# Kernel tuning notes

Hardware: AMD Instinct MI355X
Metric: run time of the kernel (lower is better)

Reference implementation:

```python
import jax, jax.numpy as jnp
import numpy as np

NB, DM, DIN, DS, DTR, K = 4, 64, 128, 16, 4, 4
C, COUT, H, W, BATCH, NH = 256, 256, 32, 32, 4, 8


def layernorm(x, w, b, eps=1e-5):
    mu = x.mean(-1, keepdims=True)
    var = ((x - mu) ** 2).mean(-1, keepdims=True)
    return (x - mu) * jax.lax.rsqrt(var + eps) * w + b


def ln_hw(x, eps=1e-5):
    # F.layer_norm(x, [H, W]) -> normalize over last two dims, no affine
    mu = x.mean((-2, -1), keepdims=True)
    var = ((x - mu) ** 2).mean((-2, -1), keepdims=True)
    return (x - mu) * jax.lax.rsqrt(var + eps)


def conv1d(x, w, b, groups=1, pad=1):
    # x: (B, Cin, L), w: (Cout, Cin//groups, k)
    y = jax.lax.conv_general_dilated(x, w, (1,), [(pad, pad)],
                                     dimension_numbers=('NCH', 'OIH', 'NCH'),
                                     feature_group_count=groups)
    return y + b[None, :, None]


def selective_scan(u, dt, Bm, Cm, A, Dp):
    # u, dt: (B,L,din); Bm, Cm: (B,L,ds); A: (din,ds); Dp: (din,)
    dA = jnp.exp(dt[..., None] * A)                     # (B,L,din,ds)
    dBu = (dt * u)[..., None] * Bm[:, :, None, :]       # (B,L,din,ds)

    def step(h, inp):
        dA_t, dBu_t, C_t = inp
        h = dA_t * h + dBu_t
        return h, jnp.einsum('bds,bs->bd', h, C_t)

    h0 = jnp.zeros((u.shape[0], DIN, DS), u.dtype)
    _, ys = jax.lax.scan(step, h0, (dA.transpose(1, 0, 2, 3), dBu.transpose(1, 0, 2, 3), Cm.transpose(1, 0, 2)))
    return ys.transpose(1, 0, 2) + u * Dp


def mamba(xs, inw, convw, convb, xpw, dtw, dtb, alog, dp, outw):
    # xs: (B,L,DM) one branch of Mamba(d_model=DM, d_state=DS, d_conv=K, expand=2)
    xz = xs @ inw.T                                     # (B,L,2*DIN)
    u, z = jnp.split(xz, 2, axis=-1)
    # causal depthwise conv1d (torch pads K-1 and truncates to L == left pad K-1)
    uc = jax.lax.conv_general_dilated(u.transpose(0, 2, 1), convw[:, None, :], (1,), [(K - 1, 0)],
                                      dimension_numbers=('NCH', 'OIH', 'NCH'),
                                      feature_group_count=DIN) + convb[None, :, None]
    u = jax.nn.silu(uc.transpose(0, 2, 1))              # (B,L,DIN)
    xdbc = u @ xpw.T                                    # (B,L,DTR+2*DS)
    dt = jax.nn.softplus(xdbc[..., :DTR] @ dtw.T + dtb)
    Bm, Cm = xdbc[..., DTR:DTR + DS], xdbc[..., DTR + DS:]
    y = selective_scan(u, dt, Bm, Cm, -jnp.exp(alog), dp)
    return (y * jax.nn.silu(z)) @ outw.T


mamba_v = jax.vmap(mamba)  # over branch axis 0 of inputs and all params


def mha(x, inw, inb, outw, outb):
    B, N, Cc = x.shape
    hd = Cc // NH
    qkv = x @ inw.T + inb
    q, k, v = jnp.split(qkv, 3, axis=-1)
    q = q.reshape(B, N, NH, hd).transpose(0, 2, 1, 3)
    k = k.reshape(B, N, NH, hd).transpose(0, 2, 1, 3)
    v = v.reshape(B, N, NH, hd).transpose(0, 2, 1, 3)
    att = jax.nn.softmax((q @ k.transpose(0, 1, 3, 2)) * (1.0 / (hd ** 0.5)), axis=-1)
    o = (att @ v).transpose(0, 2, 1, 3).reshape(B, N, Cc)
    return o @ outw.T + outb


def reference(x, norm_w, norm_b, skip_scale, m_inw, m_convw, m_convb, m_xpw, m_dtw, m_dtb, m_alog, m_d, m_outw, qdw_w, qdw_b, qpw_w, qpw_b, rdw_w, rdw_b, rpw_w, rpw_b, fdw_w, fdw_b, fpw_w, fpw_b, lc_w, lc_b, attn_inw, attn_inb, attn_outw, attn_outb, lgn_w, lgn_b, fc_w, fc_b, dwc_w, dwc_b, proj_w, proj_b):
    B, Cc, Hh, Ww = x.shape
    N = Hh * Ww
    xs = x.reshape(B, Cc, N).transpose(0, 2, 1)         # (B,N,C)
    xn = layernorm(xs, norm_w, norm_b)
    # channel-chunk into NB branches: (NB,B,N,DM)
    xc = xn.reshape(B, N, NB, DM).transpose(2, 0, 1, 3)
    xm = mamba_v(xc, m_inw, m_convw, m_convb, m_xpw, m_dtw, m_dtb, m_alog, m_d, m_outw) + skip_scale * xc
    x_concat = xm.transpose(1, 2, 0, 3).reshape(B, N, Cc)
    # branch gating: depthwise grouped conv (C->NB) then pointwise (NB->NB)
    Q = conv1d(conv1d(x_concat.transpose(0, 2, 1), qdw_w, qdw_b, groups=NB, pad=1), qpw_w, qpw_b, groups=1, pad=0)
    g = jax.nn.sigmoid(Q)                               # (B,NB,N)
    xg = (g.transpose(1, 0, 2)[..., None] * xm).transpose(1, 2, 0, 3).reshape(B, N, Cc)
    xgt = xg.transpose(0, 2, 1)                          # (B,C,N)
    R = conv1d(conv1d(xgt, rdw_w, rdw_b, groups=Cc, pad=1), rpw_w, rpw_b, groups=1, pad=0) + xgt
    cat = jnp.concatenate([xs, R.transpose(0, 2, 1)], axis=-1).transpose(0, 2, 1)  # (B,2C,N)
    xm2 = conv1d(conv1d(cat, fdw_w, fdw_b, groups=2 * Cc, pad=1), fpw_w, fpw_b, groups=1, pad=0) + cat[:, :Cc, :]
    xm2 = xm2.transpose(0, 2, 1)                         # (B,N,C)
    # local-global feature mixing
    x_local = conv1d(xm2.transpose(0, 2, 1), lc_w, lc_b, groups=Cc, pad=1).transpose(0, 2, 1)
    x_global = mha(xm2, attn_inw, attn_inb, attn_outw, attn_outb)
    x_out = jnp.concatenate([x_local, x_global], axis=-1) @ fc_w.T + fc_b
    x_out = jax.nn.gelu(layernorm(x_out, lgn_w, lgn_b), approximate=False)
    # DepthwiseConvolution: layer_norm over [H,W] (no affine) then depthwise conv2d
    xi = x_out.transpose(0, 2, 1).reshape(B, Cc, Hh, Ww)
    xi = ln_hw(xi)
    xi = jax.lax.conv_general_dilated(xi, dwc_w, (1, 1), [(1, 1), (1, 1)],
                                      dimension_numbers=('NCHW', 'OIHW', 'NCHW'),
                                      feature_group_count=Cc) + dwc_b[None, :, None, None]
    x_mixed = xi.reshape(B, Cc, N).transpose(0, 2, 1)
    x_mixed = layernorm(x_mixed, norm_w, norm_b)        # self.norm reused
    x_mixed = x_mixed @ proj_w.T + proj_b
    return x_mixed.transpose(0, 2, 1).reshape(B, COUT, Hh, Ww)


def setup_inputs() -> dict:
    key = jax.random.key(0)
    ks = iter(jax.random.split(key, 64))

    def rn(shape, s=0.02):
        return jax.random.normal(next(ks), shape, jnp.float32) * s

    return dict(
        x=jax.random.normal(next(ks), (BATCH, C, H, W), jnp.float32),
        norm_w=jnp.ones((C,), jnp.float32), norm_b=jnp.zeros((C,), jnp.float32),
        skip_scale=jnp.ones((1,), jnp.float32),
        m_inw=rn((NB, 2 * DIN, DM)), m_convw=rn((NB, DIN, K), 0.2), m_convb=jnp.zeros((NB, DIN), jnp.float32),
        m_xpw=rn((NB, DTR + 2 * DS, DIN)), m_dtw=rn((NB, DIN, DTR), 0.2), m_dtb=rn((NB, DIN), 0.5),
        m_alog=jnp.tile(jnp.log(jnp.arange(1, DS + 1, dtype=jnp.float32)), (NB, DIN, 1)),
        m_d=jnp.ones((NB, DIN), jnp.float32), m_outw=rn((NB, DM, DIN)),
        qdw_w=rn((NB, C // NB, 3), 0.1), qdw_b=jnp.zeros((NB,), jnp.float32),
        qpw_w=rn((NB, NB, 1), 0.3), qpw_b=jnp.zeros((NB,), jnp.float32),
        rdw_w=rn((C, 1, 3), 0.2), rdw_b=jnp.zeros((C,), jnp.float32),
        rpw_w=rn((C, C, 1)), rpw_b=jnp.zeros((C,), jnp.float32),
        fdw_w=rn((2 * C, 1, 3), 0.2), fdw_b=jnp.zeros((2 * C,), jnp.float32),
        fpw_w=rn((C, 2 * C, 1)), fpw_b=jnp.zeros((C,), jnp.float32),
        lc_w=rn((C, 1, 3), 0.2), lc_b=jnp.zeros((C,), jnp.float32),
        attn_inw=rn((3 * C, C)), attn_inb=jnp.zeros((3 * C,), jnp.float32),
        attn_outw=rn((C, C)), attn_outb=jnp.zeros((C,), jnp.float32),
        lgn_w=jnp.ones((C,), jnp.float32), lgn_b=jnp.zeros((C,), jnp.float32),
        fc_w=rn((C, 2 * C)), fc_b=jnp.zeros((C,), jnp.float32),
        dwc_w=rn((C, 1, 3, 3), 0.2), dwc_b=jnp.zeros((C,), jnp.float32),
        proj_w=rn((COUT, C)), proj_b=jnp.zeros((COUT,), jnp.float32),
    )
```

## Files before the change

kernel.cpp:

```cpp
#include <hip/hip_runtime.h>
#include <math.h>


namespace {
constexpr int NB_ = 4, DM_ = 64, DIN_ = 128, DS_ = 16, DTR_ = 4;
constexpr int C_ = 256, N_ = 1024, B_ = 4, HD_ = 32;
constexpr int NCH = 16, LCH = 64;
constexpr int NSTATE = 16 * 128 * 16;
}

typedef __attribute__((ext_vector_type(8))) short bf16x8;
typedef __attribute__((ext_vector_type(4))) float f32x4;
typedef __attribute__((ext_vector_type(8))) unsigned short ushort8v;
typedef __attribute__((ext_vector_type(4))) unsigned short ushort4v;

__device__ __forceinline__ unsigned short f2b(float f) {
  unsigned int u = __float_as_uint(f);
  unsigned int r = u + 0x7FFFu + ((u >> 16) & 1u);
  return (unsigned short)(r >> 16);
}

__device__ __forceinline__ float2 blockReduce2(float a, float b, float* red) {
#pragma unroll
  for (int m = 1; m < 64; m <<= 1) {
    a += __shfl_xor(a, m, 64);
    b += __shfl_xor(b, m, 64);
  }
  int w = threadIdx.x >> 6;
  if ((threadIdx.x & 63) == 0) { red[2 * w] = a; red[2 * w + 1] = b; }
  __syncthreads();
  float ra = red[0] + red[2] + red[4] + red[6];
  float rb = red[1] + red[3] + red[5] + red[7];
  return make_float2(ra, rb);
}

__device__ __forceinline__ float siluf(float x) { return x / (1.f + expf(-x)); }
__device__ __forceinline__ float sigmf(float x) { return 1.f / (1.f + expf(-x)); }
__device__ __forceinline__ float softplusf(float x) {
  return fmaxf(x, 0.f) + log1pf(expf(-fabsf(x)));
}

__global__ __launch_bounds__(256) void k_ln_t2(const float* __restrict__ in,
                                               const float* __restrict__ w,
                                               const float* __restrict__ bias,
                                               float* __restrict__ out_ln,
                                               float* __restrict__ out_copy) {
  __shared__ float tile[256][17];
  __shared__ float redp[16][16][2];
  __shared__ float stats[16][2];
  int bx = blockIdx.x;
  int b = bx >> 6, n0 = (bx & 63) * 16;
  int c = threadIdx.x;
  {
    const float* p = in + ((long)(b * C_ + c)) * N_ + n0;
#pragma unroll
    for (int j = 0; j < 16; ++j) tile[c][j] = p[j];
  }
  __syncthreads();
  {
    int n = c & 15, g = c >> 4;
    float a = 0.f, q = 0.f;
#pragma unroll
    for (int i = 0; i < 16; ++i) {
      float v = tile[g * 16 + i][n];
      a += v; q += v * v;
    }
    redp[g][n][0] = a; redp[g][n][1] = q;
  }
  __syncthreads();
  if (c < 16) {
    float a = 0.f, q = 0.f;
#pragma unroll
    for (int g2 = 0; g2 < 16; ++g2) { a += redp[g2][c][0]; q += redp[g2][c][1]; }
    float mu = a * (1.f / C_);
    float rs = rsqrtf(q * (1.f / C_) - mu * mu + 1e-5f);
    stats[c][0] = mu; stats[c][1] = rs;
  }
  __syncthreads();
  float wv = w[c], bv = bias[c];
#pragma unroll
  for (int j = 0; j < 16; ++j) {
    float v = tile[c][j];
    long o = ((long)(b * N_ + n0 + j)) * C_ + c;
    if (out_copy) out_copy[o] = v;
    out_ln[o] = (v - stats[j][0]) * stats[j][1] * wv + bv;
  }
}

__global__ __launch_bounds__(256) void k_inproj_mfma(const float* __restrict__ xn,
                                                     const float* __restrict__ inw,
                                                     float* __restrict__ UPRE,
                                                     float* __restrict__ Z) {
  __shared__ unsigned short xa[64][72];
  __shared__ unsigned short wb[64][72];
  int r0 = blockIdx.x * 64;
  int nb = blockIdx.y >> 2, c0 = (blockIdx.y & 3) * 64;
  int t = threadIdx.x;
  int wv = t >> 6, lane = t & 63, g = lane >> 4, ql = lane & 15;
  const f32x4 zf = {0.f, 0.f, 0.f, 0.f};
  f32x4 acc[4] = {zf, zf, zf, zf};
  int rr = t >> 2, kq = (t & 3) * 16;
  {
    const float* xsrc = xn + (long)(r0 + rr) * C_ + nb * 64 + kq;
#pragma unroll
    for (int j = 0; j < 4; ++j) {
      float4 v = *(const float4*)(xsrc + 4 * j);
      ushort4v u = {f2b(v.x), f2b(v.y), f2b(v.z), f2b(v.w)};
      *(ushort4v*)&xa[rr][kq + 4 * j] = u;
    }
    const float* wsrc = inw + ((long)nb * 256 + c0 + rr) * 64 + kq;
#pragma unroll
    for (int j = 0; j < 4; ++j) {
      float4 v = *(const float4*)(wsrc + 4 * j);
      ushort4v u = {f2b(v.x), f2b(v.y), f2b(v.z), f2b(v.w)};
      *(ushort4v*)&wb[rr][kq + 4 * j] = u;
    }
  }
  __syncthreads();
#pragma unroll
  for (int ks = 0; ks < 2; ++ks) {
    bf16x8 a = *(const bf16x8*)&xa[wv * 16 + ql][ks * 32 + g * 8];
#pragma unroll
    for (int ct = 0; ct < 4; ++ct) {
      bf16x8 b = *(const bf16x8*)&wb[ct * 16 + ql][ks * 32 + g * 8];
      acc[ct] = __builtin_amdgcn_mfma_f32_16x16x32_bf16(a, b, acc[ct], 0, 0, 0);
    }
  }
#pragma unroll
  for (int ct = 0; ct < 4; ++ct) {
    int col = c0 + ct * 16 + ql;
#pragma unroll
    for (int reg = 0; reg < 4; ++reg) {
      long row = (long)nb * 4096 + r0 + wv * 16 + g * 4 + reg;
      if (col < 128) UPRE[row * DIN_ + col] = acc[ct][reg];
      else           Z[row * DIN_ + col - 128] = acc[ct][reg];
    }
  }
}

__global__ __launch_bounds__(256) void k_causal(const float* __restrict__ Uin,
                                                float* __restrict__ Uout,
                                                const float* __restrict__ cw,
                                                const float* __restrict__ cb) {
  __shared__ float u_s[35][128];
  int bx = blockIdx.x;
  int nbb = bx >> 5, chk = bx & 31;
  int nb = nbb >> 2;
  int n0 = chk * 32;
  const float* ibase = Uin + (long)nbb * N_ * DIN_;
  float* obase = Uout + (long)nbb * N_ * DIN_;
  for (int i = threadIdx.x; i < 35 * 32; i += 256) {
    int row = i >> 5, q = i & 31;
    int n = n0 - 3 + row;
    float4 v = (n >= 0) ? *(const float4*)&ibase[(long)n * DIN_ + q * 4]
                        : make_float4(0.f, 0.f, 0.f, 0.f);
    *(float4*)&u_s[row][q * 4] = v;
  }
  __syncthreads();
  int d = threadIdx.x & 127, half = threadIdx.x >> 7;
  float w0 = cw[(nb * DIN_ + d) * 4 + 0], w1 = cw[(nb * DIN_ + d) * 4 + 1];
  float w2 = cw[(nb * DIN_ + d) * 4 + 2], w3 = cw[(nb * DIN_ + d) * 4 + 3];
  float bv = cb[nb * DIN_ + d];
#pragma unroll
  for (int j = 0; j < 16; ++j) {
    int nn = half * 16 + j;
    float acc = bv + w3 * u_s[nn + 3][d] + w2 * u_s[nn + 2][d] +
                w1 * u_s[nn + 1][d] + w0 * u_s[nn][d];
    obase[(long)(n0 + nn) * DIN_ + d] = siluf(acc);
  }
}

__global__ __launch_bounds__(256) void k_xdbc_mfma(const float* __restrict__ U,
                                                   const float* __restrict__ xpw,
                                                   const float* __restrict__ dtw,
                                                   const float* __restrict__ dtb,
                                                   float* __restrict__ DT,
                                                   float* __restrict__ BMb,
                                                   float* __restrict__ CMb) {
  __shared__ unsigned short xa[64][72];
  __shared__ unsigned short wb[48][72];
  __shared__ float xd_s[64][40];
  __shared__ float dtw_s[128][4];
  __shared__ float dtb_s[128];
  int t = threadIdx.x;
  long row0 = (long)blockIdx.x * 64;
  int nb = blockIdx.x >> 6;
  for (int i = t; i < 512; i += 256) dtw_s[i >> 2][i & 3] = dtw[nb * 512 + i];
  if (t < 128) dtb_s[t] = dtb[nb * DIN_ + t];
  int wv = t >> 6, lane = t & 63, g = lane >> 4, ql = lane & 15;
  const f32x4 zf = {0.f, 0.f, 0.f, 0.f};
  f32x4 acc[3] = {zf, zf, zf};
  int rr = t >> 2, kq = (t & 3) * 16;
  for (int k0 = 0; k0 < 128; k0 += 64) {
    __syncthreads();
    const float* xsrc = U + (row0 + rr) * DIN_ + k0 + kq;
#pragma unroll
    for (int j = 0; j < 4; ++j) {
      float4 v = *(const float4*)(xsrc + 4 * j);
      ushort4v u = {f2b(v.x), f2b(v.y), f2b(v.z), f2b(v.w)};
      *(ushort4v*)&xa[rr][kq + 4 * j] = u;
    }
    if (rr < 48) {
      if (rr < 36) {
        const float* wsrc = xpw + (long)nb * 36 * 128 + rr * 128 + k0 + kq;
#pragma unroll
        for (int j = 0; j < 4; ++j) {
          float4 v = *(const float4*)(wsrc + 4 * j);
          ushort4v u = {f2b(v.x), f2b(v.y), f2b(v.z), f2b(v.w)};
          *(ushort4v*)&wb[rr][kq + 4 * j] = u;
        }
      } else {
        ushort4v z = {0, 0, 0, 0};
#pragma unroll
        for (int j = 0; j < 4; ++j) *(ushort4v*)&wb[rr][kq + 4 * j] = z;
      }
    }
    __syncthreads();
#pragma unroll
    for (int ks = 0; ks < 2; ++ks) {
      bf16x8 a = *(const bf16x8*)&xa[wv * 16 + ql][ks * 32 + g * 8];
#pragma unroll
      for (int ct = 0; ct < 3; ++ct) {
        bf16x8 b = *(const bf16x8*)&wb[ct * 16 + ql][ks * 32 + g * 8];
        acc[ct] = __builtin_amdgcn_mfma_f32_16x16x32_bf16(a, b, acc[ct], 0, 0, 0);
      }
    }
  }
#pragma unroll
  for (int ct = 0; ct < 3; ++ct) {
    int col = ct * 16 + ql;
    if (col < 36) {
#pragma unroll
      for (int reg = 0; reg < 4; ++reg)
        xd_s[wv * 16 + g * 4 + reg][col] = acc[ct][reg];
    }
  }
  __syncthreads();
  {
    int r = t >> 2, sq = (t & 3) * 4;
    float4 bm4 = make_float4(xd_s[r][4 + sq], xd_s[r][5 + sq],
                             xd_s[r][6 + sq], xd_s[r][7 + sq]);
    *(float4*)&BMb[(row0 + r) * DS_ + sq] = bm4;
    float4 cm4 = make_float4(xd_s[r][20 + sq], xd_s[r][21 + sq],
                             xd_s[r][22 + sq], xd_s[r][23 + sq]);
    *(float4*)&CMb[(row0 + r) * DS_ + sq] = cm4;
  }
  {
    int r = t >> 2, dg = t & 3;
    float x0 = xd_s[r][0], x1 = xd_s[r][1], x2 = xd_s[r][2], x3 = xd_s[r][3];
    float* dst = DT + (row0 + r) * DIN_ + dg * 32;
#pragma unroll
    for (int j = 0; j < 8; ++j) {
      float o[4];
#pragma unroll
      for (int e = 0; e < 4; ++e) {
        int d = dg * 32 + j * 4 + e;
        float a = dtb_s[d] + x0 * dtw_s[d][0] + x1 * dtw_s[d][1] +
                  x2 * dtw_s[d][2] + x3 * dtw_s[d][3];
        o[e] = softplusf(a);
      }
      *(float4*)(dst + j * 4) = make_float4(o[0], o[1], o[2], o[3]);
    }
  }
}

__global__ __launch_bounds__(256) void k_scanA(const float* __restrict__ DT,
                                               const float* __restrict__ U,
                                               const float* __restrict__ BMb,
                                               const float* __restrict__ alog,
                                               float* __restrict__ Aprod,
                                               float* __restrict__ Hend) {
  __shared__ float dt_s[64][64];
  __shared__ float u_s[64][64];
  __shared__ float bm_s[64][16];
  int bx = blockIdx.x;
  int chunk = bx >> 5, rem = bx & 31, nbb = rem >> 1, dh = rem & 1;
  int nb = nbb >> 2;
  int t = threadIdx.x;
  int dl = t >> 2, sg = t & 3;
  int d = dh * 64 + dl;
  long base = (long)nbb * N_ + chunk * LCH;
#pragma unroll
  for (int j = 0; j < 4; ++j) {
    int f = t + 256 * j;
    int tt = f >> 4, dq = (f & 15) * 4;
    long src = (base + tt) * DIN_ + dh * 64 + dq;
    *(float4*)&dt_s[tt][dq] = *(const float4*)&DT[src];
    *(float4*)&u_s[tt][dq]  = *(const float4*)&U[src];
  }
  {
    int tt = t >> 2, sq = (t & 3) * 4;
    *(float4*)&bm_s[tt][sq] = *(const float4*)&BMb[(base + tt) * DS_ + sq];
  }
  float A[4];
#pragma unroll
  for (int i = 0; i < 4; ++i)
    A[i] = -expf(alog[(nb * DIN_ + d) * DS_ + sg * 4 + i]);
  __syncthreads();
  float h[4] = {0.f, 0.f, 0.f, 0.f};
  float ap[4] = {1.f, 1.f, 1.f, 1.f};
  for (int tt = 0; tt < LCH; ++tt) {
    float dtv = dt_s[tt][dl];
    float uv  = u_s[tt][dl];
    float cc = dtv * uv;
    float4 bm4 = *(const float4*)&bm_s[tt][sg * 4];
    float bmv[4] = {bm4.x, bm4.y, bm4.z, bm4.w};
#pragma unroll
    for (int i = 0; i < 4; ++i) {
      float dA = __expf(dtv * A[i]);
      h[i] = dA * h[i] + cc * bmv[i];
      ap[i] *= dA;
    }
  }
  long st = (long)chunk * NSTATE + ((nbb << 7) + d) * 16 + sg * 4;
  *(float4*)&Aprod[st] = make_float4(ap[0], ap[1], ap[2], ap[3]);
  *(float4*)&Hend[st]  = make_float4(h[0], h[1], h[2], h[3]);
}

__global__ __launch_bounds__(256) void k_scanB(float* __restrict__ Aprod,
                                               const float* __restrict__ Hend) {
  int state = blockIdx.x * 256 + threadIdx.x;
  float H = 0.f;
#pragma unroll
  for (int c = 0; c < NCH; ++c) {
    long idx = (long)c * NSTATE + state;
    float a = Aprod[idx];
    float e = Hend[idx];
    Aprod[idx] = H;
    H = e + a * H;
  }
}

__global__ __launch_bounds__(256) void k_scanC(float* __restrict__ DT,
                                               const float* __restrict__ U,
                                               const float* __restrict__ BMb,
                                               const float* __restrict__ CMb,
                                               const float* __restrict__ alog,
                                               const float* __restrict__ Dp,
                                               const float* __restrict__ Hin) {
  __shared__ float dt_s[64][64];
  __shared__ float u_s[64][64];
  __shared__ float bm_s[64][16];
  __shared__ float cm_s[64][16];
  int bx = blockIdx.x;
  int chunk = bx >> 5, rem = bx & 31, nbb = rem >> 1, dh = rem & 1;
  int nb = nbb >> 2;
  int t = threadIdx.x;
  int dl = t >> 2, sg = t & 3;
  int d = dh * 64 + dl;
  long base = (long)nbb * N_ + chunk * LCH;
#pragma unroll
  for (int j = 0; j < 4; ++j) {
    int f = t + 256 * j;
    int tt = f >> 4, dq = (f & 15) * 4;
    long src = (base + tt) * DIN_ + dh * 64 + dq;
    *(float4*)&dt_s[tt][dq] = *(const float4*)&DT[src];
    *(float4*)&u_s[tt][dq]  = *(const float4*)&U[src];
  }
  {
    int tt = t >> 2, sq = (t & 3) * 4;
    *(float4*)&bm_s[tt][sq] = *(const float4*)&BMb[(base + tt) * DS_ + sq];
    *(float4*)&cm_s[tt][sq] = *(const float4*)&CMb[(base + tt) * DS_ + sq];
  }
  float A[4];
#pragma unroll
  for (int i = 0; i < 4; ++i)
    A[i] = -expf(alog[(nb * DIN_ + d) * DS_ + sg * 4 + i]);
  float Dv = Dp[nb * DIN_ + d];
  float h[4];
  {
    long st = (long)chunk * NSTATE + ((nbb << 7) + d) * 16 + sg * 4;
    float4 h4 = *(const float4*)&Hin[st];
    h[0] = h4.x; h[1] = h4.y; h[2] = h4.z; h[3] = h4.w;
  }
  __syncthreads();
  for (int tt = 0; tt < LCH; ++tt) {
    float dtv = dt_s[tt][dl];
    float uv  = u_s[tt][dl];
    float cc = dtv * uv;
    float4 bm4 = *(const float4*)&bm_s[tt][sg * 4];
    float4 cm4 = *(const float4*)&cm_s[tt][sg * 4];
    float bmv[4] = {bm4.x, bm4.y, bm4.z, bm4.w};
    float cmv[4] = {cm4.x, cm4.y, cm4.z, cm4.w};
    float p = 0.f;
#pragma unroll
    for (int i = 0; i < 4; ++i) {
      float dA = __expf(dtv * A[i]);
      h[i] = dA * h[i] + cc * bmv[i];
      p += h[i] * cmv[i];
    }
    p += __shfl_xor(p, 1, 64);
    p += __shfl_xor(p, 2, 64);
    if (sg == 0) DT[(base + tt) * DIN_ + d] = p + Dv * uv;
  }
}

__global__ __launch_bounds__(256) void k_outproj_mfma(const float* __restrict__ Y,
                                                      const float* __restrict__ Zb,
                                                      const float* __restrict__ outw,
                                                      const float* __restrict__ xn,
                                                      const float* __restrict__ skip,
                                                      float* __restrict__ XMC) {
  __shared__ unsigned short xa[64][72];
  __shared__ unsigned short wb[64][72];
  int r0 = blockIdx.x * 64;
  int nb = blockIdx.y;
  int t = threadIdx.x;
  int wv = t >> 6, lane = t & 63, g = lane >> 4, ql = lane & 15;
  const f32x4 zf = {0.f, 0.f, 0.f, 0.f};
  f32x4 acc[4] = {zf, zf, zf, zf};
  int rr = t >> 2, kq = (t & 3) * 16;
  for (int k0 = 0; k0 < 128; k0 += 64) {
    __syncthreads();
    long row = (long)nb * 4096 + r0 + rr;
    const float* ysrc = Y + row * DIN_ + k0 + kq;
    const float* zsrc = Zb + row * DIN_ + k0 + kq;
#pragma unroll
    for (int j = 0; j < 4; ++j) {
      float4 yv = *(const float4*)(ysrc + 4 * j);
      float4 zv = *(const float4*)(zsrc + 4 * j);
      ushort4v u = {f2b(yv.x * siluf(zv.x)), f2b(yv.y * siluf(zv.y)),
                    f2b(yv.z * siluf(zv.z)), f2b(yv.w * siluf(zv.w))};
      *(ushort4v*)&xa[rr][kq + 4 * j] = u;
    }
    const float* wsrc = outw + ((long)nb * 64 + rr) * 128 + k0 + kq;
#pragma unroll
    for (int j = 0; j < 4; ++j) {
      float4 v = *(const float4*)(wsrc + 4 * j);
      ushort4v u = {f2b(v.x), f2b(v.y), f2b(v.z), f2b(v.w)};
      *(ushort4v*)&wb[rr][kq + 4 * j] = u;
    }
    __syncthreads();
#pragma unroll
    for (int ks = 0; ks < 2; ++ks) {
      bf16x8 a = *(const bf16x8*)&xa[wv * 16 + ql][ks * 32 + g * 8];
#pragma unroll
      for (int ct = 0; ct < 4; ++ct) {
        bf16x8 b = *(const bf16x8*)&wb[ct * 16 + ql][ks * 32 + g * 8];
        acc[ct] = __builtin_amdgcn_mfma_f32_16x16x32_bf16(a, b, acc[ct], 0, 0, 0);
      }
    }
  }
  float sk = skip[0];
#pragma unroll
  for (int ct = 0; ct < 4; ++ct) {
    int col = ct * 16 + ql;
#pragma unroll
    for (int reg = 0; reg < 4; ++reg) {
      int bn = r0 + wv * 16 + g * 4 + reg;
      long oc = (long)bn * C_ + nb * 64 + col;
      XMC[oc] = acc[ct][reg] + sk * xn[oc];
    }
  }
}

__global__ __launch_bounds__(256) void k_gate(const float* __restrict__ XMC,
                                              const float* __restrict__ qdw_w,
                                              const float* __restrict__ qdw_b,
                                              const float* __restrict__ qpw_w,
                                              const float* __restrict__ qpw_b,
                                              float* __restrict__ G) {
  int t = threadIdx.x;
  int gid = (blockIdx.x * 256 + t) >> 4;
  int cq = t & 3, p = (t >> 2) & 3;
  int b = gid >> 10, n = gid & 1023;
  float a = 0.f;
#pragma unroll
  for (int k = 0; k < 3; ++k) {
    int nn = n + k - 1;
    if (nn < 0 || nn >= N_) continue;
    const float* xr = XMC + ((long)b * N_ + nn) * C_ + p * 64 + cq * 16;
    const float* wr = qdw_w + (p * 64 + cq * 16) * 3 + k;
#pragma unroll
    for (int i = 0; i < 16; ++i) a += xr[i] * wr[i * 3];
  }
  a += __shfl_xor(a, 1, 64);
  a += __shfl_xor(a, 2, 64);
  float q1 = a + qdw_b[p];
  int lane = t & 63;
  float q1g[4];
#pragma unroll
  for (int pp = 0; pp < 4; ++pp) q1g[pp] = __shfl(q1, (lane & ~12) | (pp << 2), 64);
  int o = p;
  float r = qpw_b[o];
#pragma unroll
  for (int pp = 0; pp < 4; ++pp) r += qpw_w[o * 4 + pp] * q1g[pp];
  if (cq == 0) G[((long)b * 4 + o) * N_ + n] = sigmf(r);
}

__global__ __launch_bounds__(256) void k_xg(const float* __restrict__ XMC,
                                            const float* __restrict__ G,
                                            float* __restrict__ XG) {
  __shared__ float tile[64][65];
  int bx = blockIdx.x;
  int b = bx >> 6, ct = (bx >> 4) & 3, nt = bx & 15;
  int c0 = ct * 64, n0 = nt * 64;
  int t = threadIdx.x;
  {
    int cc = t & 63, nq = t >> 6;
#pragma unroll
    for (int j = 0; j < 16; ++j) {
      int nn = nq * 16 + j;
      tile[cc][nn] = XMC[((long)(b * N_ + n0 + nn)) * C_ + c0 + cc];
    }
  }
  __syncthreads();
  {
    int nl = t & 63, cq = t >> 6;
    float g = G[((long)(b * 4 + ct)) * N_ + n0 + nl];
#pragma unroll
    for (int j = 0; j < 16; ++j) {
      int cl = cq * 16 + j;
      XG[((long)(b * C_ + c0 + cl)) * N_ + n0 + nl] = g * tile[cl][nl];
    }
  }
}

template <int KD>
__global__ __launch_bounds__(256) void k_gemm_cm_dw(const float* __restrict__ inA,
                                                    const float* __restrict__ inB,
                                                    const float* __restrict__ dww,
                                                    const float* __restrict__ dwb,
                                                    const float* __restrict__ w,
                                                    const float* __restrict__ bias,
                                                    const float* __restrict__ residCM,
                                                    const float* __restrict__ residRM,
                                                    float* __restrict__ outCM,
                                                    float* __restrict__ outRM) {
  __shared__ unsigned short xa[64][72];
  __shared__ unsigned short wb[64][72];
  int rb = blockIdx.x;
  int b = rb >> 4, n0 = (rb & 15) * 64;
  int c0 = blockIdx.y * 64;
  int t = threadIdx.x;
  int wv = t >> 6, lane = t & 63, g = lane >> 4, ql = lane & 15;
  const f32x4 zf = {0.f, 0.f, 0.f, 0.f};
  f32x4 acc[4] = {zf, zf, zf, zf};
  int rr = t >> 2, kq = (t & 3) * 16;
  for (int k0 = 0; k0 < KD; k0 += 64) {
    __syncthreads();
    {
      int k = k0 + rr;
      const float* src = (inB != nullptr && k >= 256)
                             ? inB + ((long)(b * 256 + k - 256)) * 1024
                             : inA + ((long)(b * 256 + k)) * 1024;
      float w0 = dww[k * 3], w1 = dww[k * 3 + 1], w2 = dww[k * 3 + 2], bv = dwb[k];
#pragma unroll
      for (int j = 0; j < 4; ++j) {
        int nb4 = n0 + kq + 4 * j;
        float4 v = *(const float4*)&src[nb4];
        float vm1 = (nb4 > 0) ? src[nb4 - 1] : 0.f;
        float vp4 = (nb4 + 4 < 1024) ? src[nb4 + 4] : 0.f;
        xa[kq + 4 * j + 0][rr] = f2b(bv + w0 * vm1 + w1 * v.x + w2 * v.y);
        xa[kq + 4 * j + 1][rr] = f2b(bv + w0 * v.x + w1 * v.y + w2 * v.z);
        xa[kq + 4 * j + 2][rr] = f2b(bv + w0 * v.y + w1 * v.z + w2 * v.w);
        xa[kq + 4 * j + 3][rr] = f2b(bv + w0 * v.z + w1 * v.w + w2 * vp4);
      }
    }
    const float* wsrc = w + (long)(c0 + rr) * KD + k0 + kq;
#pragma unroll
    for (int j = 0; j < 4; ++j) {
      float4 v = *(const float4*)(wsrc + 4 * j);
      ushort4v u = {f2b(v.x), f2b(v.y), f2b(v.z), f2b(v.w)};
      *(ushort4v*)&wb[rr][kq + 4 * j] = u;
    }
    __syncthreads();
#pragma unroll
    for (int ks = 0; ks < 2; ++ks) {
      bf16x8 a = *(const bf16x8*)&xa[wv * 16 + ql][ks * 32 + g * 8];
#pragma unroll
      for (int ct = 0; ct < 4; ++ct) {
        bf16x8 bfr = *(const bf16x8*)&wb[ct * 16 + ql][ks * 32 + g * 8];
        acc[ct] = __builtin_amdgcn_mfma_f32_16x16x32_bf16(a, bfr, acc[ct], 0, 0, 0);
      }
    }
  }
#pragma unroll
  for (int ct = 0; ct < 4; ++ct) {
    int col = c0 + ct * 16 + ql;
    float bv = bias[col];
    if (outCM) {
      long base = ((long)(b * 256 + col)) * 1024 + n0 + wv * 16 + g * 4;
      float4 r4 = *(const float4*)(residCM + base);
      float4 o = make_float4(acc[ct][0] + bv + r4.x, acc[ct][1] + bv + r4.y,
                             acc[ct][2] + bv + r4.z, acc[ct][3] + bv + r4.w);
      *(float4*)(outCM + base) = o;
    } else {
#pragma unroll
      for (int reg = 0; reg < 4; ++reg) {
        long row = (long)b * 1024 + n0 + wv * 16 + g * 4 + reg;
        long idx = row * 256 + col;
        outRM[idx] = acc[ct][reg] + bv + residRM[idx];
      }
    }
  }
}

template <int KD>
__global__ __launch_bounds__(256) void k_gemm_rm(const float* __restrict__ inA,
                                                 const float* __restrict__ w,
                                                 const float* __restrict__ bias,
                                                 float* __restrict__ out, int Cout) {
  __shared__ unsigned short xa[64][72];
  __shared__ unsigned short wb[64][72];
  int r0 = blockIdx.x * 64;
  int c0 = blockIdx.y * 64;
  int t = threadIdx.x;
  int wv = t >> 6, lane = t & 63, g = lane >> 4, ql = lane & 15;
  const f32x4 zf = {0.f, 0.f, 0.f, 0.f};
  f32x4 acc[4] = {zf, zf, zf, zf};
  int rr = t >> 2, kq = (t & 3) * 16;
  for (int k0 = 0; k0 < KD; k0 += 64) {
    __syncthreads();
    int kk = k0 + kq;
    const float* xsrc = inA + (long)(r0 + rr) * KD + kk;
#pragma unroll
    for (int j = 0; j < 4; ++j) {
      float4 v = *(const float4*)(xsrc + 4 * j);
      ushort4v u = {f2b(v.x), f2b(v.y), f2b(v.z), f2b(v.w)};
      *(ushort4v*)&xa[rr][kq + 4 * j] = u;
    }
    const float* wsrc = w + (long)(c0 + rr) * KD + kk;
#pragma unroll
    for (int j = 0; j < 4; ++j) {
      float4 v = *(const float4*)(wsrc + 4 * j);
      ushort4v u = {f2b(v.x), f2b(v.y), f2b(v.z), f2b(v.w)};
      *(ushort4v*)&wb[rr][kq + 4 * j] = u;
    }
    __syncthreads();
#pragma unroll
    for (int ks = 0; ks < 2; ++ks) {
      bf16x8 a = *(const bf16x8*)&xa[wv * 16 + ql][ks * 32 + g * 8];
#pragma unroll
      for (int ct = 0; ct < 4; ++ct) {
        bf16x8 b = *(const bf16x8*)&wb[ct * 16 + ql][ks * 32 + g * 8];
        acc[ct] = __builtin_amdgcn_mfma_f32_16x16x32_bf16(a, b, acc[ct], 0, 0, 0);
      }
    }
  }
#pragma unroll
  for (int ct = 0; ct < 4; ++ct) {
    int col = c0 + ct * 16 + ql;
    float bv = bias[col];
#pragma unroll
    for (int reg = 0; reg < 4; ++reg) {
      long row = r0 + wv * 16 + g * 4 + reg;
      out[row * Cout + col] = acc[ct][reg] + bv;
    }
  }
}

__global__ __launch_bounds__(256) void k_gemm_qkv(const float* __restrict__ in,
                                                  const float* __restrict__ w,
                                                  const float* __restrict__ bias,
                                                  unsigned short* __restrict__ out) {
  __shared__ unsigned short xa[64][72];
  __shared__ unsigned short wb[64][72];
  int r0 = blockIdx.x * 64;
  int c0 = blockIdx.y * 64;
  int t = threadIdx.x;
  int wv = t >> 6, lane = t & 63, g = lane >> 4, ql = lane & 15;
  const f32x4 zf = {0.f, 0.f, 0.f, 0.f};
  f32x4 acc[4] = {zf, zf, zf, zf};
  int rr = t >> 2, kq = (t & 3) * 16;
  for (int k0 = 0; k0 < 256; k0 += 64) {
    __syncthreads();
    const float* xsrc = in + (long)(r0 + rr) * 256 + k0 + kq;
#pragma unroll
    for (int j = 0; j < 4; ++j) {
      float4 v = *(const float4*)(xsrc + 4 * j);
      ushort4v u = {f2b(v.x), f2b(v.y), f2b(v.z), f2b(v.w)};
      *(ushort4v*)&xa[rr][kq + 4 * j] = u;
    }
    const float* wsrc = w + (long)(c0 + rr) * 256 + k0 + kq;
#pragma unroll
    for (int j = 0; j < 4; ++j) {
// ... 111 lines not shown
  int g = lane >> 4, ql = lane & 15;
  const float qscale = 0.17677669529663687f * 1.44269504088896341f;

  bf16x8 q_frag = *(const bf16x8*)(qkvb + ((long)(b * N_ + qt * 64 + w * 16 + ql)) * 768 + h * HD_ + g * 8);
  float m = -1e30f, l = 0.f;
  f32x4 o_acc[2];
  const f32x4 zf = {0.f, 0.f, 0.f, 0.f};
  o_acc[0] = zf; o_acc[1] = zf;

  for (int kt = 0; kt < 16; ++kt) {
    __syncthreads();
    {
      int kr = t >> 2, d0 = (t & 3) * 8;
      const unsigned short* gp = qkvb + ((long)(b * N_ + kt * 64 + kr)) * 768 + 256 + h * HD_ + d0;
      ushort8v kv = *(const ushort8v*)gp;
      *(ushort8v*)&K_lds[kr * 40 + d0] = kv;
      ushort8v vv = *(const ushort8v*)(gp + 256);
#pragma unroll
      for (int i = 0; i < 8; ++i) Vt_lds[(d0 + i) * 72 + kr] = vv[i];
    }
    __syncthreads();
    f32x4 s_frag[4];
#pragma unroll
    for (int s = 0; s < 4; ++s) {
      bf16x8 k_frag = *(const bf16x8*)&K_lds[(s * 16 + ql) * 40 + g * 8];
      s_frag[s] = __builtin_amdgcn_mfma_f32_16x16x32_bf16(k_frag, q_frag, zf, 0, 0, 0);
    }
    float sv[16];
#pragma unroll
    for (int s = 0; s < 4; ++s)
#pragma unroll
      for (int r = 0; r < 4; ++r) sv[s * 4 + r] = s_frag[s][r] * qscale;
    float tmax = sv[0];
#pragma unroll
    for (int i = 1; i < 16; ++i) tmax = fmaxf(tmax, sv[i]);
    tmax = fmaxf(tmax, __shfl_xor(tmax, 16));
    tmax = fmaxf(tmax, __shfl_xor(tmax, 32));
    float mn = fmaxf(m, tmax);
    float corr = exp2f(m - mn);
    float psum = 0.f;
    unsigned short pb[16];
#pragma unroll
    for (int i = 0; i < 16; ++i) {
      float p = exp2f(sv[i] - mn);
      psum += p;
      pb[i] = f2b(p);
    }
    psum += __shfl_xor(psum, 16);
    psum += __shfl_xor(psum, 32);
    l = l * corr + psum;
    m = mn;
#pragma unroll
    for (int mt = 0; mt < 2; ++mt)
#pragma unroll
      for (int r = 0; r < 4; ++r) o_acc[mt][r] *= corr;
#pragma unroll
    for (int s = 0; s < 4; ++s) {
      ushort4v p4 = {pb[s * 4], pb[s * 4 + 1], pb[s * 4 + 2], pb[s * 4 + 3]};
      *(ushort4v*)&P_lds[w][ql * 72 + s * 16 + g * 4] = p4;
    }
#pragma unroll
    for (int c = 0; c < 2; ++c) {
      bf16x8 p_frag = *(const bf16x8*)&P_lds[w][ql * 72 + c * 32 + g * 8];
#pragma unroll
      for (int mt = 0; mt < 2; ++mt) {
        bf16x8 v_frag = *(const bf16x8*)&Vt_lds[(mt * 16 + ql) * 72 + c * 32 + g * 8];
        o_acc[mt] = __builtin_amdgcn_mfma_f32_16x16x32_bf16(v_frag, p_frag, o_acc[mt], 0, 0, 0);
      }
    }
  }
  float inv = 1.f / l;
  float* op = O + ((long)(b * N_ + qt * 64 + w * 16 + ql)) * C_ + h * HD_;
#pragma unroll
  for (int mt = 0; mt < 2; ++mt) {
    float4 o4 = make_float4(o_acc[mt][0] * inv, o_acc[mt][1] * inv,
                            o_acc[mt][2] * inv, o_acc[mt][3] * inv);
    *(float4*)(op + mt * 16 + g * 4) = o4;
  }
}

__global__ __launch_bounds__(256) void k_lngelu(const float* __restrict__ XO,
                                                const float* __restrict__ lw,
                                                const float* __restrict__ lb,
                                                float* __restrict__ XI) {
  __shared__ float tile[256][17];
  __shared__ float redp[16][16][2];
  __shared__ float stats[16][2];
  int bx = blockIdx.x;
  int b = bx >> 6, n0 = (bx & 63) * 16;
  int c = threadIdx.x;
#pragma unroll
  for (int j = 0; j < 16; ++j)
    tile[c][j] = XO[((long)(b * N_ + n0 + j)) * C_ + c];
  __syncthreads();
  {
    int n = c & 15, g = c >> 4;
    float a = 0.f, q = 0.f;
#pragma unroll
    for (int i = 0; i < 16; ++i) {
      float v = tile[g * 16 + i][n];
      a += v; q += v * v;
    }
    redp[g][n][0] = a; redp[g][n][1] = q;
  }
  __syncthreads();
  if (c < 16) {
    float a = 0.f, q = 0.f;
#pragma unroll
    for (int g2 = 0; g2 < 16; ++g2) { a += redp[g2][c][0]; q += redp[g2][c][1]; }
    float mu = a * (1.f / C_);
    float rs = rsqrtf(q * (1.f / C_) - mu * mu + 1e-5f);
    stats[c][0] = mu; stats[c][1] = rs;
  }
  __syncthreads();
  float wv = lw[c], bv = lb[c];
  float o[16];
#pragma unroll
  for (int j = 0; j < 16; ++j) {
    float x = (tile[c][j] - stats[j][0]) * stats[j][1] * wv + bv;
    o[j] = 0.5f * x * (1.f + erff(x * 0.70710678118654752f));
  }
  float* dst = &XI[((long)(b * C_ + c)) * N_ + n0];
#pragma unroll
  for (int j4 = 0; j4 < 4; ++j4)
    *(float4*)(dst + j4 * 4) = make_float4(o[4 * j4], o[4 * j4 + 1], o[4 * j4 + 2], o[4 * j4 + 3]);
}

__global__ __launch_bounds__(256) void k_lnhw_dwc(const float* __restrict__ XIin,
                                                  const float* __restrict__ w,
                                                  const float* __restrict__ bias,
                                                  float* __restrict__ XD) {
  __shared__ float pl[32][33];
  __shared__ float red[8];
  long base = (long)blockIdx.x * 1024;
  int c = blockIdx.x & 255;
  int t = threadIdx.x;
  float4 v = *(const float4*)&XIin[base + t * 4];
  float a = v.x + v.y + v.z + v.w;
  float q = v.x * v.x + v.y * v.y + v.z * v.z + v.w * v.w;
  float2 s = blockReduce2(a, q, red);
  float mu = s.x * (1.f / 1024.f);
  float rs = rsqrtf(s.y * (1.f / 1024.f) - mu * mu + 1e-5f);
  int hh = t >> 3, w0 = (t & 7) * 4;
  pl[hh][w0 + 0] = (v.x - mu) * rs;
  pl[hh][w0 + 1] = (v.y - mu) * rs;
  pl[hh][w0 + 2] = (v.z - mu) * rs;
  pl[hh][w0 + 3] = (v.w - mu) * rs;
  __syncthreads();
  float wk[9];
#pragma unroll
  for (int i = 0; i < 9; ++i) wk[i] = w[c * 9 + i];
  float bv = bias[c];
  float o[4];
#pragma unroll
  for (int j = 0; j < 4; ++j) {
    int ww = w0 + j;
    float acc = bv;
#pragma unroll
    for (int kh = 0; kh < 3; ++kh) {
      int h2 = hh + kh - 1;
      if (h2 < 0 || h2 >= 32) continue;
#pragma unroll
      for (int kw = 0; kw < 3; ++kw) {
        int w2 = ww + kw - 1;
        if (w2 < 0 || w2 >= 32) continue;
        acc += wk[kh * 3 + kw] * pl[h2][w2];
      }
    }
    o[j] = acc;
  }
  *(float4*)&XD[base + t * 4] = make_float4(o[0], o[1], o[2], o[3]);
}

__global__ __launch_bounds__(256) void k_lnproj(const float* __restrict__ XD,
                                                const float* __restrict__ nw,
                                                const float* __restrict__ nbias,
                                                const float* __restrict__ w,
                                                const float* __restrict__ bias,
                                                float* __restrict__ out) {
  __shared__ unsigned short xa[64][72];
  __shared__ unsigned short wb[64][72];
  __shared__ float ps[4][64], pq[4][64];
  __shared__ float mu_s[64], rs_s[64];
  int rb = blockIdx.x;
  int b = rb >> 4, n0 = (rb & 15) * 64;
  int c0 = blockIdx.y * 64;
  int t = threadIdx.x;
  {
    int nl = t & 63, cq = t >> 6;
    const float* src = XD + ((long)(b * 256 + cq * 64)) * 1024 + n0 + nl;
    float s = 0.f, q = 0.f;
    for (int i = 0; i < 64; ++i) {
      float v = src[(long)i * 1024];
      s += v; q += v * v;
    }
    ps[cq][nl] = s; pq[cq][nl] = q;
  }
  __syncthreads();
  if (t < 64) {
    float s = ps[0][t] + ps[1][t] + ps[2][t] + ps[3][t];
    float q = pq[0][t] + pq[1][t] + pq[2][t] + pq[3][t];
    float mu = s * (1.f / 256.f);
    float rs = rsqrtf(q * (1.f / 256.f) - mu * mu + 1e-5f);
    mu_s[t] = mu; rs_s[t] = rs;
  }
  int wv = t >> 6, lane = t & 63, g = lane >> 4, ql = lane & 15;
  const f32x4 zf = {0.f, 0.f, 0.f, 0.f};
  f32x4 acc[4] = {zf, zf, zf, zf};
  int rr = t >> 2, kq = (t & 3) * 16;
  for (int k0 = 0; k0 < 256; k0 += 64) {
    __syncthreads();
    {
      int ch = k0 + rr;
      const float* src = XD + ((long)(b * 256 + ch)) * 1024 + n0 + kq;
      float wv_ = nw[ch], bv_ = nbias[ch];
#pragma unroll
      for (int j = 0; j < 4; ++j) {
        float4 v = *(const float4*)(src + 4 * j);
        int n = kq + 4 * j;
        xa[n + 0][rr] = f2b((v.x - mu_s[n + 0]) * rs_s[n + 0] * wv_ + bv_);
        xa[n + 1][rr] = f2b((v.y - mu_s[n + 1]) * rs_s[n + 1] * wv_ + bv_);
        xa[n + 2][rr] = f2b((v.z - mu_s[n + 2]) * rs_s[n + 2] * wv_ + bv_);
        xa[n + 3][rr] = f2b((v.w - mu_s[n + 3]) * rs_s[n + 3] * wv_ + bv_);
      }
      const float* wsrc = w + (long)(c0 + rr) * 256 + k0 + kq;
#pragma unroll
      for (int j = 0; j < 4; ++j) {
        float4 v = *(const float4*)(wsrc + 4 * j);
        ushort4v u = {f2b(v.x), f2b(v.y), f2b(v.z), f2b(v.w)};
        *(ushort4v*)&wb[rr][kq + 4 * j] = u;
      }
    }
    __syncthreads();
#pragma unroll
    for (int ks = 0; ks < 2; ++ks) {
      bf16x8 a = *(const bf16x8*)&xa[wv * 16 + ql][ks * 32 + g * 8];
#pragma unroll
      for (int ct = 0; ct < 4; ++ct) {
        bf16x8 bfr = *(const bf16x8*)&wb[ct * 16 + ql][ks * 32 + g * 8];
        acc[ct] = __builtin_amdgcn_mfma_f32_16x16x32_bf16(a, bfr, acc[ct], 0, 0, 0);
      }
    }
  }
#pragma unroll
  for (int ct = 0; ct < 4; ++ct) {
    int col = c0 + ct * 16 + ql;
    float bv = bias[col];
    long basei = ((long)(b * 256 + col)) * 1024 + n0 + wv * 16 + g * 4;
    *(float4*)(out + basei) = make_float4(acc[ct][0] + bv, acc[ct][1] + bv,
                                          acc[ct][2] + bv, acc[ct][3] + bv);
  }
}

extern "C" void kernel_launch(void* const* d_in, const int* in_sizes, int n_in,
                              void* d_out, int out_size, void* d_ws, size_t ws_size,
                              hipStream_t stream) {
  const float* x        = (const float*)d_in[0];
  const float* norm_w   = (const float*)d_in[1];
  const float* norm_b   = (const float*)d_in[2];
  const float* skip     = (const float*)d_in[3];
  const float* m_inw    = (const float*)d_in[4];
  const float* m_convw  = (const float*)d_in[5];
  const float* m_convb  = (const float*)d_in[6];
  const float* m_xpw    = (const float*)d_in[7];
  const float* m_dtw    = (const float*)d_in[8];
  const float* m_dtb    = (const float*)d_in[9];
  const float* m_alog   = (const float*)d_in[10];
  const float* m_d      = (const float*)d_in[11];
  const float* m_outw   = (const float*)d_in[12];
  const float* qdw_w    = (const float*)d_in[13];
  const float* qdw_b    = (const float*)d_in[14];
  const float* qpw_w    = (const float*)d_in[15];
  const float* qpw_b    = (const float*)d_in[16];
  const float* rdw_w    = (const float*)d_in[17];
  const float* rdw_b    = (const float*)d_in[18];
  const float* rpw_w    = (const float*)d_in[19];
  const float* rpw_b    = (const float*)d_in[20];
  const float* fdw_w    = (const float*)d_in[21];
  const float* fdw_b    = (const float*)d_in[22];
  const float* fpw_w    = (const float*)d_in[23];
  const float* fpw_b    = (const float*)d_in[24];
  const float* lc_w     = (const float*)d_in[25];
  const float* lc_b     = (const float*)d_in[26];
  const float* attn_inw = (const float*)d_in[27];
  const float* attn_inb = (const float*)d_in[28];
  const float* attn_outw= (const float*)d_in[29];
  const float* attn_outb= (const float*)d_in[30];
  const float* lgn_w    = (const float*)d_in[31];
  const float* lgn_b    = (const float*)d_in[32];
  const float* fc_w     = (const float*)d_in[33];
  const float* fc_b     = (const float*)d_in[34];
  const float* dwc_w    = (const float*)d_in[35];
  const float* dwc_b    = (const float*)d_in[36];
  const float* proj_w   = (const float*)d_in[37];
  const float* proj_b   = (const float*)d_in[38];
  float* out = (float*)d_out;

  float* ws = (float*)d_ws;
  const size_t F = 1048576;
  float* XS  = ws + 0 * F;
  float* XN  = ws + 1 * F;
  float* U   = ws + 2 * F;
  float* Z   = ws + 4 * F;
  float* UPRE= ws + 6 * F;
  float* DT  = ws + 6 * F;
  float* BM  = ws + 8 * F;
  float* CM  = ws + 8 * F + F / 4;
  float* XMC = ws + 8 * F + F / 2;
  float* SC_APROD = ws + 8 * F + F / 2;
  float* SC_HEND  = ws + 9 * F;
  float* G   = ws + 1 * F;
  float* XG  = ws + 2 * F;
  float* RB  = ws + 4 * F;
  float* XM2 = ws + 5 * F;
  unsigned short* QKVB = (unsigned short*)(ws + 1 * F);
  float* O   = ws + 4 * F;
  float* XGL = ws + 6 * F;
  float* XO  = ws + 7 * F;
  float* XI  = ws + 8 * F;
  float* XD  = ws + 5 * F;
  (void)ws_size; (void)in_sizes; (void)n_in; (void)out_size;

  k_ln_t2<<<256, 256, 0, stream>>>(x, norm_w, norm_b, XN, XS);
  k_inproj_mfma<<<dim3(64, 16), 256, 0, stream>>>(XN, m_inw, UPRE, Z);
  k_causal<<<512, 256, 0, stream>>>(UPRE, U, m_convw, m_convb);
  k_xdbc_mfma<<<256, 256, 0, stream>>>(U, m_xpw, m_dtw, m_dtb, DT, BM, CM);
  k_scanA<<<512, 256, 0, stream>>>(DT, U, BM, m_alog, SC_APROD, SC_HEND);
  k_scanB<<<128, 256, 0, stream>>>(SC_APROD, SC_HEND);
  k_scanC<<<512, 256, 0, stream>>>(DT, U, BM, CM, m_alog, m_d, SC_APROD);
  k_outproj_mfma<<<dim3(64, 4), 256, 0, stream>>>(DT, Z, m_outw, XN, skip, XMC);
  k_gate<<<256, 256, 0, stream>>>(XMC, qdw_w, qdw_b, qpw_w, qpw_b, G);
  k_xg<<<256, 256, 0, stream>>>(XMC, G, XG);
  k_gemm_cm_dw<256><<<dim3(64, 4), 256, 0, stream>>>(XG, nullptr, rdw_w, rdw_b,
                                                     rpw_w, rpw_b, XG, nullptr, RB, nullptr);
  k_gemm_cm_dw<512><<<dim3(64, 4), 256, 0, stream>>>(x, RB, fdw_w, fdw_b,
                                                     fpw_w, fpw_b, nullptr, XS, nullptr, XM2);
  k_gemm_qkv<<<dim3(64, 12), 256, 0, stream>>>(XM2, attn_inw, attn_inb, QKVB);
  k_attn_mfma<<<512, 256, 0, stream>>>(QKVB, O);
  k_gemm_rm<256><<<dim3(64, 4), 256, 0, stream>>>(O, attn_outw, attn_outb, XGL, 256);
  k_gemm_fc<<<dim3(64, 4), 256, 0, stream>>>(XM2, XGL, lc_w, lc_b, fc_w, fc_b, XO);
  k_lngelu<<<256, 256, 0, stream>>>(XO, lgn_w, lgn_b, XI);
  k_lnhw_dwc<<<1024, 256, 0, stream>>>(XI, dwc_w, dwc_b, XD);
  k_lnproj<<<dim3(64, 4), 256, 0, stream>>>(XD, norm_w, norm_b, proj_w, proj_b, out);
}
```

Measured before the change: 209.3 us.

## Fuse causal conv into in-projection GEMM and fold chunk-prefix scan into scanC

The in-projection MFMA kernel now applies the causal depthwise conv and SiLU to the u half directly from shared memory. It recomputes the three halo rows with a scalar fp32 dot product, which removes the UPRE round-trip and the separate k_causal launch. The inter-chunk prefix kernel k_scanB is removed; each scanC block walks the preceding chunk summaries itself to build its starting state. This saves two launches and a global pass, at the cost of redundant prefix work in later chunks. The halo rows are computed in fp32 while the main tile uses bf16, a small precision mismatch.

```diff
diff --git a/kernel.cpp b/kernel.cpp
--- a/kernel.cpp
+++ b/kernel.cpp
@@ -87,14 +87,17 @@
   }
 }
 
-__global__ __launch_bounds__(256) void k_inproj_mfma(const float* __restrict__ xn,
+__global__ __launch_bounds__(256) void k_inproj_conv(const float* __restrict__ xn,
                                                      const float* __restrict__ inw,
-                                                     float* __restrict__ UPRE,
+                                                     const float* __restrict__ cw,
+                                                     const float* __restrict__ cb,
+                                                     float* __restrict__ U,
                                                      float* __restrict__ Z) {
   __shared__ unsigned short xa[64][72];
   __shared__ unsigned short wb[64][72];
+  __shared__ float ut[67][65];
   int r0 = blockIdx.x * 64;
-  int nb = blockIdx.y >> 2, c0 = (blockIdx.y & 3) * 64;
+  int nb = blockIdx.y >> 2, q = blockIdx.y & 3, c0 = q * 64;
   int t = threadIdx.x;
   int wv = t >> 6, lane = t & 63, g = lane >> 4, ql = lane & 15;
   const f32x4 zf = {0.f, 0.f, 0.f, 0.f};
@@ -126,47 +129,50 @@
       acc[ct] = __builtin_amdgcn_mfma_f32_16x16x32_bf16(a, b, acc[ct], 0, 0, 0);
     }
   }
-#pragma unroll
-  for (int ct = 0; ct < 4; ++ct) {
-    int col = c0 + ct * 16 + ql;
-#pragma unroll
-    for (int reg = 0; reg < 4; ++reg) {
-      long row = (long)nb * 4096 + r0 + wv * 16 + g * 4 + reg;
-      if (col < 128) UPRE[row * DIN_ + col] = acc[ct][reg];
-      else           Z[row * DIN_ + col - 128] = acc[ct][reg];
-    }
-  }
-}
-
-__global__ __launch_bounds__(256) void k_causal(const float* __restrict__ Uin,
-                                                float* __restrict__ Uout,
-                                                const float* __restrict__ cw,
-                                                const float* __restrict__ cb) {
-  __shared__ float u_s[35][128];
-  int bx = blockIdx.x;
-  int nbb = bx >> 5, chk = bx & 31;
-  int nb = nbb >> 2;
-  int n0 = chk * 32;
-  const float* ibase = Uin + (long)nbb * N_ * DIN_;
-  float* obase = Uout + (long)nbb * N_ * DIN_;
-  for (int i = threadIdx.x; i < 35 * 32; i += 256) {
-    int row = i >> 5, q = i & 31;
-    int n = n0 - 3 + row;
-    float4 v = (n >= 0) ? *(const float4*)&ibase[(long)n * DIN_ + q * 4]
-                        : make_float4(0.f, 0.f, 0.f, 0.f);
-    *(float4*)&u_s[row][q * 4] = v;
-  }
-  __syncthreads();
-  int d = threadIdx.x & 127, half = threadIdx.x >> 7;
-  float w0 = cw[(nb * DIN_ + d) * 4 + 0], w1 = cw[(nb * DIN_ + d) * 4 + 1];
-  float w2 = cw[(nb * DIN_ + d) * 4 + 2], w3 = cw[(nb * DIN_ + d) * 4 + 3];
-  float bv = cb[nb * DIN_ + d];
-#pragma unroll
-  for (int j = 0; j < 16; ++j) {
-    int nn = half * 16 + j;
-    float acc = bv + w3 * u_s[nn + 3][d] + w2 * u_s[nn + 2][d] +
-                w1 * u_s[nn + 1][d] + w0 * u_s[nn][d];
-    obase[(long)(n0 + nn) * DIN_ + d] = siluf(acc);
+  if (q < 2) {
+#pragma unroll
+    for (int ct = 0; ct < 4; ++ct)
+#pragma unroll
+      for (int reg = 0; reg < 4; ++reg)
+        ut[3 + wv * 16 + g * 4 + reg][ct * 16 + ql] = acc[ct][reg];
+    if (t < 192) {
+      int hr = t >> 6, lc = t & 63;
+      float hv = 0.f;
+      if ((r0 & 1023) != 0) {
+        const float* xrow = xn + (long)(r0 - 3 + hr) * C_ + nb * 64;
+        const float* wrow = inw + ((long)nb * 256 + c0 + lc) * 64;
+#pragma unroll 8
+        for (int k = 0; k < 64; ++k) hv += xrow[k] * wrow[k];
+      }
+      ut[hr][lc] = hv;
+    }
+    __syncthreads();
+#pragma unroll
+    for (int ct = 0; ct < 4; ++ct) {
+      int lc = ct * 16 + ql;
+      int d = c0 + lc;
+      const float* cwp = cw + (nb * DIN_ + d) * 4;
+      float w0 = cwp[0], w1 = cwp[1], w2 = cwp[2], w3 = cwp[3];
+      float bv = cb[nb * DIN_ + d];
+#pragma unroll
+      for (int reg = 0; reg < 4; ++reg) {
+        int lr = wv * 16 + g * 4 + reg;
+        float a = bv + w3 * ut[3 + lr][lc] + w2 * ut[2 + lr][lc] +
+                  w1 * ut[1 + lr][lc] + w0 * ut[lr][lc];
+        long row = (long)nb * 4096 + r0 + lr;
+        U[row * DIN_ + d] = siluf(a);
+      }
+    }
+  } else {
+#pragma unroll
+    for (int ct = 0; ct < 4; ++ct) {
+      int col = c0 - 128 + ct * 16 + ql;
+#pragma unroll
+      for (int reg = 0; reg < 4; ++reg) {
+        long row = (long)nb * 4096 + r0 + wv * 16 + g * 4 + reg;
+        Z[row * DIN_ + col] = acc[ct][reg];
+      }
+    }
   }
 }
 
@@ -317,27 +323,14 @@
   *(float4*)&Hend[st]  = make_float4(h[0], h[1], h[2], h[3]);
 }
 
-__global__ __launch_bounds__(256) void k_scanB(float* __restrict__ Aprod,
-                                               const float* __restrict__ Hend) {
-  int state = blockIdx.x * 256 + threadIdx.x;
-  float H = 0.f;
-#pragma unroll
-  for (int c = 0; c < NCH; ++c) {
-    long idx = (long)c * NSTATE + state;
-    float a = Aprod[idx];
-    float e = Hend[idx];
-    Aprod[idx] = H;
-    H = e + a * H;
-  }
-}
-
 __global__ __launch_bounds__(256) void k_scanC(float* __restrict__ DT,
                                                const float* __restrict__ U,
                                                const float* __restrict__ BMb,
                                                const float* __restrict__ CMb,
                                                const float* __restrict__ alog,
                                                const float* __restrict__ Dp,
-                                               const float* __restrict__ Hin) {
+                                               const float* __restrict__ Aprod,
+                                               const float* __restrict__ Hend) {
   __shared__ float dt_s[64][64];
   __shared__ float u_s[64][64];
   __shared__ float bm_s[64][16];
@@ -367,11 +360,17 @@
   for (int i = 0; i < 4; ++i)
     A[i] = -expf(alog[(nb * DIN_ + d) * DS_ + sg * 4 + i]);
   float Dv = Dp[nb * DIN_ + d];
-  float h[4];
+  float h[4] = {0.f, 0.f, 0.f, 0.f};
   {
-    long st = (long)chunk * NSTATE + ((nbb << 7) + d) * 16 + sg * 4;
-    float4 h4 = *(const float4*)&Hin[st];
-    h[0] = h4.x; h[1] = h4.y; h[2] = h4.z; h[3] = h4.w;
+    long state4 = ((nbb << 7) + d) * 16 + sg * 4;
+    for (int c = 0; c < chunk; ++c) {
+      float4 a4 = *(const float4*)&Aprod[(long)c * NSTATE + state4];
+      float4 e4 = *(const float4*)&Hend[(long)c * NSTATE + state4];
+      h[0] = e4.x + a4.x * h[0];
+      h[1] = e4.y + a4.y * h[1];
+      h[2] = e4.z + a4.z * h[2];
+      h[3] = e4.w + a4.w * h[3];
+    }
   }
   __syncthreads();
   for (int tt = 0; tt < LCH; ++tt) {
@@ -1089,7 +1088,6 @@
   float* XN  = ws + 1 * F;
   float* U   = ws + 2 * F;
   float* Z   = ws + 4 * F;
-  float* UPRE= ws + 6 * F;
   float* DT  = ws + 6 * F;
   float* BM  = ws + 8 * F;
   float* CM  = ws + 8 * F + F / 4;
@@ -1109,12 +1107,10 @@
   (void)ws_size; (void)in_sizes; (void)n_in; (void)out_size;
 
   k_ln_t2<<<256, 256, 0, stream>>>(x, norm_w, norm_b, XN, XS);
-  k_inproj_mfma<<<dim3(64, 16), 256, 0, stream>>>(XN, m_inw, UPRE, Z);
-  k_causal<<<512, 256, 0, stream>>>(UPRE, U, m_convw, m_convb);
+  k_inproj_conv<<<dim3(64, 16), 256, 0, stream>>>(XN, m_inw, m_convw, m_convb, U, Z);
   k_xdbc_mfma<<<256, 256, 0, stream>>>(U, m_xpw, m_dtw, m_dtb, DT, BM, CM);
   k_scanA<<<512, 256, 0, stream>>>(DT, U, BM, m_alog, SC_APROD, SC_HEND);
-  k_scanB<<<128, 256, 0, stream>>>(SC_APROD, SC_HEND);
-  k_scanC<<<512, 256, 0, stream>>>(DT, U, BM, CM, m_alog, m_d, SC_APROD);
+  k_scanC<<<512, 256, 0, stream>>>(DT, U, BM, CM, m_alog, m_d, SC_APROD, SC_HEND);
   k_outproj_mfma<<<dim3(64, 4), 256, 0, stream>>>(DT, Z, m_outw, XN, skip, XMC);
   k_gate<<<256, 256, 0, stream>>>(XMC, qdw_w, qdw_b, qpw_w, qpw_b, G);
   k_xg<<<256, 256, 0, stream>>>(XMC, G, XG);
```

Result: no change. 208.3 us (-0.5%).
